# Performance work log

Hardware: AMD Instinct MI355X
Metric: run time of the kernel (lower is better)

The kernel has to match this reference:

```python
import jax, jax.numpy as jnp
import numpy as np

HEADS, IN_F, OUT_F, N = 8, 256, 64, 4096


def _xavier(key, shape):
    fan_in, fan_out = shape[-2], shape[-1]
    lim = float(np.sqrt(6.0 / (fan_in + fan_out)))
    return jax.random.uniform(key, shape, jnp.float32, -lim, lim)


def setup_inputs() -> dict:
    key = jax.random.key(0)
    k1, k2, k3, k4 = jax.random.split(key, 4)
    h = jax.random.normal(k1, (N, IN_F), jnp.float32)
    adj = jax.random.uniform(k2, (N, N), jnp.float32)  # unused by forward (faithful)
    W = _xavier(k3, (HEADS, IN_F, OUT_F))
    a = _xavier(k4, (HEADS, 2 * OUT_F, 1))
    return {"h": h, "adj": adj, "W": W, "a": a}


def reference(h, adj, W, a):
    n = h.shape[0]
    heads, _, out_f = W.shape
    # h_prime: [heads, N, out]
    hp = jnp.einsum('ni,hio->hno', h, W)
    # decompose a into the two halves acting on source/target features
    a1 = a[:, :out_f, 0]   # [heads, out]
    a2 = a[:, out_f:, 0]   # [heads, out]
    e_src = jnp.einsum('hno,ho->hn', hp, a1)  # [heads, N]
    e_dst = jnp.einsum('hno,ho->hn', hp, a2)  # [heads, N]
    # e[h,i,j] = a1.hp_i + a2.hp_j  (no leakyrelu, no adj mask: faithful to source)
    e = e_src[:, :, None] + e_dst[:, None, :]  # [heads, N, N]
    attention = jax.nn.softmax(e, axis=-1)
    h_out = jnp.einsum('hij,hjo->hio', attention, hp)  # [heads, N, out]
    # faithful to torch .view(N, -1) on contiguous [heads, N, out]
    return h_out.reshape(n, heads * out_f)
```

## Files before the change

kernel.cpp:

```cpp
#include <hip/hip_runtime.h>
#include <hip/hip_bf16.h>


#define HEADS 8
#define IN_F 256
#define OUT_F 64
#define NN 4096
#define ECHUNKS 16
#define GCHUNKS 32
#define GROWS (NN / GCHUNKS)

__global__ void k_edst(const float* __restrict__ hmat,
                       const float* __restrict__ W,
                       const float* __restrict__ a,
                       float* __restrict__ e_dst) {
    const int blk   = blockIdx.x;
    const int head  = blk >> 4;
    const int chunk = blk & (ECHUNKS - 1);
    const int tid   = threadIdx.x;

    __shared__ float a2[OUT_F];
    __shared__ float v[IN_F];

    if (tid < OUT_F) a2[tid] = a[head * 2 * OUT_F + OUT_F + tid];
    __syncthreads();

    {
        const float4* Wr = reinterpret_cast<const float4*>(
            W + (size_t)(head * IN_F + tid) * OUT_F);
        float acc = 0.f;
#pragma unroll
        for (int o4 = 0; o4 < OUT_F / 4; ++o4) {
            float4 w4 = Wr[o4];
            acc += w4.x * a2[o4 * 4 + 0] + w4.y * a2[o4 * 4 + 1] +
                   w4.z * a2[o4 * 4 + 2] + w4.w * a2[o4 * 4 + 3];
        }
        v[tid] = acc;
    }
    __syncthreads();

    const int n = chunk * 256 + tid;
    const float4* hr = reinterpret_cast<const float4*>(hmat + (size_t)n * IN_F);
    float acc = 0.f;
#pragma unroll 8
    for (int k4 = 0; k4 < IN_F / 4; ++k4) {
        float4 h4 = hr[k4];
        acc += h4.x * v[k4 * 4 + 0] + h4.y * v[k4 * 4 + 1] +
               h4.z * v[k4 * 4 + 2] + h4.w * v[k4 * 4 + 3];
    }
    e_dst[head * NN + n] = acc;
}

__global__ void k_gpart(const float* __restrict__ hmat,
                        const float* __restrict__ e_dst,
                        float* __restrict__ g_part) {
    const int blk   = blockIdx.x;
    const int head  = blk >> 5;
    const int chunk = blk & (GCHUNKS - 1);
    const int tid   = threadIdx.x;

    __shared__ float red[256];
    __shared__ float wts[GROWS];

    const float* e = e_dst + head * NN;

    float m = -INFINITY;
    for (int i = tid; i < NN; i += 256) m = fmaxf(m, e[i]);
    red[tid] = m;
    __syncthreads();
    for (int s = 128; s > 0; s >>= 1) {
        if (tid < s) red[tid] = fmaxf(red[tid], red[tid + s]);
        __syncthreads();
    }
    m = red[0];
    __syncthreads();

    float ssum = 0.f;
    for (int i = tid; i < NN; i += 256) ssum += __expf(e[i] - m);
    red[tid] = ssum;
    __syncthreads();
    for (int s = 128; s > 0; s >>= 1) {
        if (tid < s) red[tid] += red[tid + s];
        __syncthreads();
    }
    const float inv = 1.f / red[0];

    if (tid < GROWS)
        wts[tid] = __expf(e[chunk * GROWS + tid] - m) * inv;
    __syncthreads();

    const float* hb = hmat + (size_t)chunk * GROWS * IN_F;
    float acc = 0.f;
#pragma unroll 4
    for (int j = 0; j < GROWS; ++j)
        acc += wts[j] * hb[(size_t)j * IN_F + tid];
    g_part[(size_t)(head * GCHUNKS + chunk) * IN_F + tid] = acc;
}

__global__ void k_outrow(const float* __restrict__ W,
                         const float* __restrict__ g_part,
                         float* __restrict__ out_row) {
    const int head = blockIdx.x;
    const int tid  = threadIdx.x;

    __shared__ float g[IN_F];
    __shared__ float part[256];

    float acc = 0.f;
    for (int c = 0; c < GCHUNKS; ++c)
        acc += g_part[(size_t)(head * GCHUNKS + c) * IN_F + tid];
    g[tid] = acc;
    __syncthreads();

    const int o = tid & 63, grp = tid >> 6;
    float p = 0.f;
#pragma unroll 4
    for (int kk = 0; kk < 64; ++kk) {
        int k = grp * 64 + kk;
        p += g[k] * W[(size_t)(head * IN_F + k) * OUT_F + o];
    }
    part[tid] = p;
    __syncthreads();
    if (tid < 64)
        out_row[head * OUT_F + tid] =
            part[tid] + part[tid + 64] + part[tid + 128] + part[tid + 192];
}

__global__ void k_bcast(const float* __restrict__ out_row,
                        float4* __restrict__ out) {
    __shared__ float4 r[HEADS * OUT_F / 4];
    const int tid = threadIdx.x;
    if (tid < HEADS * OUT_F / 4)
        r[tid] = reinterpret_cast<const float4*>(out_row)[tid];
    __syncthreads();
    const size_t idx = (size_t)blockIdx.x * 256 + tid;
    const int head = (int)(idx >> 16);
    const int o4   = (int)(idx & 15);
    out[idx] = r[head * 16 + o4];
}

extern "C" void kernel_launch(void* const* d_in, const int* in_sizes, int n_in,
                              void* d_out, int out_size, void* d_ws, size_t ws_size,
                              hipStream_t stream) {
    const float* hmat = (const float*)d_in[0];
    const float* W = (const float*)d_in[2];
    const float* a = (const float*)d_in[3];
    float* out = (float*)d_out;
    float* ws  = (float*)d_ws;

    float* e_dst   = ws;
    float* g_part  = e_dst + HEADS * NN;
    float* out_row = g_part + HEADS * GCHUNKS * IN_F;

    k_edst  <<<HEADS * ECHUNKS, 256, 0, stream>>>(hmat, W, a, e_dst);
    k_gpart <<<HEADS * GCHUNKS, 256, 0, stream>>>(hmat, e_dst, g_part);
    k_outrow<<<HEADS,           256, 0, stream>>>(W, g_part, out_row);
    k_bcast <<<2048,            256, 0, stream>>>(out_row, (float4*)out);
}
```

Baseline: 126.4 us.

## Fuse output-row computation with broadcast and use wavefront shuffle reductions

Merges the per-head output-row kernel and the broadcast kernel into one kernel of 512 blocks. Each block recomputes its head's row from the partial sums and writes 1024 float4s, which removes one launch and the round trip through the row buffer. The softmax max/sum reductions in the partial kernel now use 64-lane shuffles plus a 4-entry shared combine instead of a shared-memory tree with many barriers. The cost is that each head's row is now recomputed redundantly in 64 blocks, each re-reading g_part and W.

```diff
diff --git a/kernel.cpp b/kernel.cpp
--- a/kernel.cpp
+++ b/kernel.cpp
@@ -59,31 +59,26 @@
     const int chunk = blk & (GCHUNKS - 1);
     const int tid   = threadIdx.x;
 
-    __shared__ float red[256];
+    __shared__ float wredm[4], wreds[4];
     __shared__ float wts[GROWS];
 
     const float* e = e_dst + head * NN;
 
     float m = -INFINITY;
     for (int i = tid; i < NN; i += 256) m = fmaxf(m, e[i]);
-    red[tid] = m;
+#pragma unroll
+    for (int off = 32; off > 0; off >>= 1) m = fmaxf(m, __shfl_xor(m, off));
+    if ((tid & 63) == 0) wredm[tid >> 6] = m;
     __syncthreads();
-    for (int s = 128; s > 0; s >>= 1) {
-        if (tid < s) red[tid] = fmaxf(red[tid], red[tid + s]);
-        __syncthreads();
-    }
-    m = red[0];
-    __syncthreads();
+    m = fmaxf(fmaxf(wredm[0], wredm[1]), fmaxf(wredm[2], wredm[3]));
 
     float ssum = 0.f;
     for (int i = tid; i < NN; i += 256) ssum += __expf(e[i] - m);
-    red[tid] = ssum;
+#pragma unroll
+    for (int off = 32; off > 0; off >>= 1) ssum += __shfl_xor(ssum, off);
+    if ((tid & 63) == 0) wreds[tid >> 6] = ssum;
     __syncthreads();
-    for (int s = 128; s > 0; s >>= 1) {
-        if (tid < s) red[tid] += red[tid + s];
-        __syncthreads();
-    }
-    const float inv = 1.f / red[0];
+    const float inv = 1.f / (wreds[0] + wreds[1] + wreds[2] + wreds[3]);
 
     if (tid < GROWS)
         wts[tid] = __expf(e[chunk * GROWS + tid] - m) * inv;
@@ -97,16 +92,19 @@
     g_part[(size_t)(head * GCHUNKS + chunk) * IN_F + tid] = acc;
 }
 
-__global__ void k_outrow(const float* __restrict__ W,
+__global__ void k_rowout(const float* __restrict__ W,
                          const float* __restrict__ g_part,
-                         float* __restrict__ out_row) {
-    const int head = blockIdx.x;
+                         float4* __restrict__ out) {
+    const int blk  = blockIdx.x;
+    const int head = blk >> 6;
     const int tid  = threadIdx.x;
 
     __shared__ float g[IN_F];
     __shared__ float part[256];
+    __shared__ float row[OUT_F];
 
     float acc = 0.f;
+#pragma unroll 8
     for (int c = 0; c < GCHUNKS; ++c)
         acc += g_part[(size_t)(head * GCHUNKS + c) * IN_F + tid];
     g[tid] = acc;
@@ -121,22 +119,17 @@
     }
     part[tid] = p;
     __syncthreads();
-    if (tid < 64)
-        out_row[head * OUT_F + tid] =
-            part[tid] + part[tid + 64] + part[tid + 128] + part[tid + 192];
-}
+    if (tid < OUT_F)
+        row[tid] = part[tid] + part[tid + 64] + part[tid + 128] + part[tid + 192];
+    __syncthreads();
 
-__global__ void k_bcast(const float* __restrict__ out_row,
-                        float4* __restrict__ out) {
-    __shared__ float4 r[HEADS * OUT_F / 4];
-    const int tid = threadIdx.x;
-    if (tid < HEADS * OUT_F / 4)
-        r[tid] = reinterpret_cast<const float4*>(out_row)[tid];
-    __syncthreads();
-    const size_t idx = (size_t)blockIdx.x * 256 + tid;
-    const int head = (int)(idx >> 16);
-    const int o4   = (int)(idx & 15);
-    out[idx] = r[head * 16 + o4];
+    const float4* r4 = reinterpret_cast<const float4*>(row);
+    const size_t base = (size_t)blk * 1024;
+#pragma unroll
+    for (int j = 0; j < 4; ++j) {
+        size_t idx = base + (size_t)j * 256 + tid;
+        out[idx] = r4[idx & 15];
+    }
 }
 
 extern "C" void kernel_launch(void* const* d_in, const int* in_sizes, int n_in,
@@ -148,12 +141,10 @@
     float* out = (float*)d_out;
     float* ws  = (float*)d_ws;
 
-    float* e_dst   = ws;
-    float* g_part  = e_dst + HEADS * NN;
-    float* out_row = g_part + HEADS * GCHUNKS * IN_F;
+    float* e_dst  = ws;
+    float* g_part = e_dst + HEADS * NN;
 
     k_edst  <<<HEADS * ECHUNKS, 256, 0, stream>>>(hmat, W, a, e_dst);
     k_gpart <<<HEADS * GCHUNKS, 256, 0, stream>>>(hmat, e_dst, g_part);
-    k_outrow<<<HEADS,           256, 0, stream>>>(W, g_part, out_row);
-    k_bcast <<<2048,            256, 0, stream>>>(out_row, (float4*)out);
+    k_rowout<<<512,             256, 0, stream>>>(W, g_part, (float4*)out);
 }
```

Result: no change. 124.9 us (-1.2%).
